# Kernel tuning notes

Measured on AMD Instinct MI355X. Metric: run time of the kernel, lower is better.

## Reference

```python
import jax, jax.numpy as jnp
import numpy as np

DIM = 512
N_HEADS = 8
HEAD_DIM = DIM // N_HEADS


def rope_pos(T, head_dim, dtype=jnp.float32):
    inv_freq = 1.0 / (10000.0 ** (jnp.arange(0, head_dim, 2, dtype=jnp.float32) / head_dim))
    t = jnp.arange(T, dtype=jnp.float32)
    freqs = jnp.einsum('i,j->ij', t, inv_freq)            # [T, head_dim/2]
    return jnp.concatenate([freqs, freqs], axis=-1).astype(dtype)  # [T, head_dim]


def rotate_half(x):
    x1, x2 = jnp.split(x, 2, axis=-1)
    return jnp.concatenate([-x2, x1], axis=-1)


def apply_rope(pos, t):
    # pos: [T, hd] -> broadcast to [1,1,T,hd]; t: [B,H,T,hd]
    pos = pos[None, None, :, :]
    return t * jnp.cos(pos) + rotate_half(t) * jnp.sin(pos)


def setup_inputs() -> dict:
    key = jax.random.key(0)
    ks = jax.random.split(key, 6)
    B, T = 4, 2048
    x = jax.random.normal(ks[0], (B, T, DIM), dtype=jnp.float32)
    mask = jnp.zeros((B, T), dtype=jnp.float32)  # additive mask
    s = 1.0 / np.sqrt(DIM)
    qkv_w = jax.random.normal(ks[1], (3 * DIM, DIM), dtype=jnp.float32) * s
    qkv_b = jnp.zeros((3 * DIM,), dtype=jnp.float32)
    proj_w = jax.random.normal(ks[2], (DIM, DIM), dtype=jnp.float32) * s
    proj_b = jnp.zeros((DIM,), dtype=jnp.float32)
    return {"x": x, "mask": mask, "qkv_w": qkv_w, "qkv_b": qkv_b,
            "proj_w": proj_w, "proj_b": proj_b}


def reference(x, mask, qkv_w, qkv_b, proj_w, proj_b):
    B, T, C = x.shape
    qkv = x @ qkv_w.T + qkv_b                       # [B,T,3C]
    qkv = qkv.reshape(B, T, 3, N_HEADS, HEAD_DIM)
    q, k, v = qkv[:, :, 0], qkv[:, :, 1], qkv[:, :, 2]  # [B,T,H,hd]
    q = q.transpose(0, 2, 1, 3)                     # [B,H,T,hd]
    k = k.transpose(0, 2, 1, 3)
    v = v.transpose(0, 2, 1, 3)
    pos = rope_pos(T, HEAD_DIM, x.dtype)
    q = apply_rope(pos, q)
    k = apply_rope(pos, k)
    scores = jnp.einsum('bhqd,bhkd->bhqk', q, k) * (1.0 / np.sqrt(HEAD_DIM))
    scores = scores + mask[:, None, None, :]        # 2D mask -> [B,1,1,T]
    probs = jax.nn.softmax(scores.astype(jnp.float32), axis=-1).astype(x.dtype)
    # dropout is identity in eval mode
    out = jnp.einsum('bhqk,bhkd->bhqd', probs, v)   # [B,H,T,hd]
    out = out.transpose(0, 2, 1, 3).reshape(B, T, C)
    return out @ proj_w.T + proj_b
```

## Files before the change

### kernel.cpp

```cpp
#include <hip/hip_runtime.h>
#include <math.h>


typedef __attribute__((ext_vector_type(8))) short bf16x8;
typedef __attribute__((ext_vector_type(4))) float floatx4;

#define LOG2E 1.44269504088896f

__device__ __forceinline__ unsigned short f2bf(float f) {
  unsigned int u = __float_as_uint(f);
  u += 0x7fffu + ((u >> 16) & 1u);
  return (unsigned short)(u >> 16);
}

__device__ __forceinline__ unsigned int cvtpk_bf16(float a, float b) {
  unsigned int r;
  asm("v_cvt_pk_bf16_f32 %0, %1, %2" : "=v"(r) : "v"(a), "v"(b));
  return r;
}

__device__ __forceinline__ void gld_lds16(unsigned short* lds, const unsigned short* g) {
  __builtin_amdgcn_global_load_lds(
      (const __attribute__((address_space(1))) unsigned int*)g,
      (__attribute__((address_space(3))) unsigned int*)lds, 16, 0, 0);
}

__global__ __launch_bounds__(256) void prep_kernel(
    const float* __restrict__ x, const float* __restrict__ wq, const float* __restrict__ wp,
    unsigned short* __restrict__ xb, unsigned short* __restrict__ wqb,
    unsigned short* __restrict__ wpb, float* __restrict__ cosT, float* __restrict__ sinT) {
  int i = blockIdx.x * 256 + threadIdx.x;
  if (i < 4194304) {
    xb[i] = f2bf(x[i]);
  } else if (i < 4980736) {
    int j = i - 4194304; wqb[j] = f2bf(wq[j]);
  } else if (i < 5242880) {
    int j = i - 4980736; wpb[j] = f2bf(wp[j]);
  } else if (i < 5308416) {
    int j = i - 5242880;
    int t = j >> 5, f = j & 31;
    double fr = (double)t * pow(10000.0, -(double)f / 32.0);
    cosT[j] = (float)cos(fr);
    sinT[j] = (float)sin(fr);
  }
}

__global__ __launch_bounds__(256) void qkv_kernel(
    const unsigned short* __restrict__ xb, const unsigned short* __restrict__ wqb,
    const float* __restrict__ qkv_b, const float* __restrict__ cosT,
    const float* __restrict__ sinT, unsigned short* __restrict__ Qb,
    unsigned short* __restrict__ Kb, unsigned short* __restrict__ Vtb) {
  __shared__ __align__(16) unsigned short As[128 * 32];
  __shared__ __align__(16) unsigned short Bs[128 * 32];
  const int tid = threadIdx.x;
  const int wave = tid >> 6, lane = tid & 63, ln = lane & 15, quad = lane >> 4;
  const int m0 = blockIdx.x * 128, n0 = blockIdx.y * 128;
  const int wr = (wave >> 1) * 64, wc = (wave & 1) * 64;

  floatx4 acc[4][4];
#pragma unroll
  for (int i = 0; i < 4; ++i)
#pragma unroll
    for (int j = 0; j < 4; ++j) acc[i][j] = (floatx4){0.f, 0.f, 0.f, 0.f};

  const int c0 = tid, c1 = tid + 256;
  const int ar0 = c0 >> 2, ak0 = (c0 & 3) * 8;
  const int ar1 = c1 >> 2, ak1 = (c1 & 3) * 8;

  for (int k0 = 0; k0 < 512; k0 += 32) {
    __syncthreads();
    gld_lds16(As + c0 * 8, xb + (size_t)(m0 + ar0) * 512 + k0 + ak0);
    gld_lds16(As + c1 * 8, xb + (size_t)(m0 + ar1) * 512 + k0 + ak1);
    gld_lds16(Bs + c0 * 8, wqb + (size_t)(n0 + ar0) * 512 + k0 + ak0);
    gld_lds16(Bs + c1 * 8, wqb + (size_t)(n0 + ar1) * 512 + k0 + ak1);
    __syncthreads();
    bf16x8 af[4], bfb[4];
#pragma unroll
    for (int mi = 0; mi < 4; ++mi)
      af[mi] = *(const bf16x8*)(As + (wr + mi * 16 + ln) * 32 + quad * 8);
#pragma unroll
    for (int ni = 0; ni < 4; ++ni)
      bfb[ni] = *(const bf16x8*)(Bs + (wc + ni * 16 + ln) * 32 + quad * 8);
#pragma unroll
    for (int mi = 0; mi < 4; ++mi)
#pragma unroll
      for (int ni = 0; ni < 4; ++ni)
        acc[mi][ni] = __builtin_amdgcn_mfma_f32_16x16x32_bf16(af[mi], bfb[ni], acc[mi][ni], 0, 0, 0);
  }

  const int colbase = n0 + wc;
  const int mat = colbase >> 9;
  const int h = (colbase & 511) >> 6;
  float bias[4];
#pragma unroll
  for (int ni = 0; ni < 4; ++ni) bias[ni] = qkv_b[colbase + ni * 16 + ln];

  if (mat == 2) {
#pragma unroll
    for (int mi = 0; mi < 4; ++mi) {
      int row0 = m0 + wr + mi * 16 + quad * 4;
      int bidx = row0 >> 11, t = row0 & 2047;
#pragma unroll
      for (int ni = 0; ni < 4; ++ni) {
        int d = ni * 16 + ln;
        ushort4 pk;
        pk.x = f2bf(acc[mi][ni][0] + bias[ni]);
        pk.y = f2bf(acc[mi][ni][1] + bias[ni]);
        pk.z = f2bf(acc[mi][ni][2] + bias[ni]);
        pk.w = f2bf(acc[mi][ni][3] + bias[ni]);
        *(ushort4*)(Vtb + ((size_t)(bidx * 8 + h) * 64 + d) * 2048 + t) = pk;
      }
    }
  } else {
    unsigned short* dst = (mat == 0) ? Qb : Kb;
    const float sc = (mat == 0) ? 0.125f * LOG2E : 1.0f;
#pragma unroll
    for (int mi = 0; mi < 4; ++mi) {
#pragma unroll
      for (int r = 0; r < 4; ++r) {
        int row = m0 + wr + mi * 16 + quad * 4 + r;
        int bidx = row >> 11, t = row & 2047;
        const float* cr = cosT + t * 32;
        const float* sr = sinT + t * 32;
        size_t obase = ((size_t)(bidx * 8 + h) * 2048 + t) * 64;
#pragma unroll
        for (int ni = 0; ni < 2; ++ni) {
          int dlo = ni * 16 + ln;
          float cv = cr[dlo], sv = sr[dlo];
          float xlo = acc[mi][ni][r] + bias[ni];
          float xhi = acc[mi][ni + 2][r] + bias[ni + 2];
          dst[obase + dlo]      = f2bf((xlo * cv - xhi * sv) * sc);
          dst[obase + dlo + 32] = f2bf((xhi * cv + xlo * sv) * sc);
        }
      }
    }
  }
}

__global__ __launch_bounds__(512) void attn_kernel(
    const unsigned short* __restrict__ Qb, const unsigned short* __restrict__ Kb,
    const unsigned short* __restrict__ Vtb, const float* __restrict__ mask,
    unsigned short* __restrict__ attnb) {
  __shared__ __align__(16) unsigned short Ks[64 * 64];
  __shared__ __align__(16) unsigned short Vs[64 * 64];
  __shared__ __align__(16) unsigned short Ps[128 * 64];

  const int tid = threadIdx.x;
  const int wave = tid >> 6, lane = tid & 63, ln = lane & 15, quad = lane >> 4;
  const int swz = (ln & 7) << 3;
  const int bh = blockIdx.y;
  const int b = bh >> 3, h = bh & 7;
  const int q0 = blockIdx.x * 128;
  const int wq = wave * 16;

  const unsigned short* Qhead = Qb + (size_t)bh * 2048 * 64;
  const unsigned short* Khead = Kb + (size_t)bh * 2048 * 64;
  const unsigned short* Vhead = Vtb + (size_t)bh * 64 * 2048;

  bf16x8 qf[2];
#pragma unroll
  for (int ks = 0; ks < 2; ++ks)
    qf[ks] = *(const bf16x8*)(Qhead + (size_t)(q0 + wq + ln) * 64 + ks * 32 + quad * 8);

  floatx4 o[4];
#pragma unroll
  for (int mi2 = 0; mi2 < 4; ++mi2) o[mi2] = (floatx4){0.f, 0.f, 0.f, 0.f};
  float mrun = -INFINITY;
  float lrun = 0.f;

  const int srow = tid >> 3;
  const int scol = (tid & 7) * 8;
  const int sdst = srow * 64 + (scol ^ ((srow & 7) << 3));
  uint4 kpre = *(const uint4*)(Khead + (size_t)srow * 64 + scol);
  uint4 vpre = *(const uint4*)(Vhead + (size_t)srow * 2048 + scol);

  for (int k0 = 0; k0 < 2048; k0 += 64) {
    __syncthreads();
    *(uint4*)(Ks + sdst) = kpre;
    *(uint4*)(Vs + sdst) = vpre;
    __syncthreads();
    if (k0 + 64 < 2048) {
      kpre = *(const uint4*)(Khead + (size_t)(k0 + 64 + srow) * 64 + scol);
      vpre = *(const uint4*)(Vhead + (size_t)srow * 2048 + k0 + 64 + scol);
    }

    floatx4 sm[4];
#pragma unroll
    for (int mi = 0; mi < 4; ++mi) {
      bf16x8 kf0 = *(const bf16x8*)(Ks + (mi * 16 + ln) * 64 + ((quad * 8) ^ swz));
      bf16x8 kf1 = *(const bf16x8*)(Ks + (mi * 16 + ln) * 64 + ((32 + quad * 8) ^ swz));
      floatx4 a = (floatx4){0.f, 0.f, 0.f, 0.f};
      a = __builtin_amdgcn_mfma_f32_16x16x32_bf16(kf0, qf[0], a, 0, 0, 0);
      a = __builtin_amdgcn_mfma_f32_16x16x32_bf16(kf1, qf[1], a, 0, 0, 0);
      sm[mi] = a;
    }
#pragma unroll
    for (int mi = 0; mi < 4; ++mi) {
      float4 mv = *(const float4*)(mask + b * 2048 + k0 + mi * 16 + quad * 4);
      sm[mi][0] += mv.x * LOG2E; sm[mi][1] += mv.y * LOG2E;
      sm[mi][2] += mv.z * LOG2E; sm[mi][3] += mv.w * LOG2E;
    }
    float vmax = fmaxf(fmaxf(sm[0][0], sm[0][1]), fmaxf(sm[0][2], sm[0][3]));
#pragma unroll
    for (int mi = 1; mi < 4; ++mi)
      vmax = fmaxf(vmax, fmaxf(fmaxf(sm[mi][0], sm[mi][1]), fmaxf(sm[mi][2], sm[mi][3])));
    vmax = fmaxf(vmax, __shfl_xor(vmax, 16));
    vmax = fmaxf(vmax, __shfl_xor(vmax, 32));
    if (__any(vmax > mrun)) {
      float nm = fmaxf(mrun, vmax);
      float alpha = exp2f(mrun - nm);
      mrun = nm;
      lrun *= alpha;
#pragma unroll
      for (int mi2 = 0; mi2 < 4; ++mi2) {
        o[mi2][0] *= alpha; o[mi2][1] *= alpha;
        o[mi2][2] *= alpha; o[mi2][3] *= alpha;
      }
    }
    float psum = 0.f;
#pragma unroll
    for (int mi = 0; mi < 4; ++mi)
#pragma unroll
      for (int r = 0; r < 4; ++r) {
        float p = exp2f(sm[mi][r] - mrun);
        sm[mi][r] = p;
        psum += p;
      }
    psum += __shfl_xor(psum, 16);
    psum += __shfl_xor(psum, 32);
    lrun += psum;

#pragma unroll
    for (int mi = 0; mi < 4; ++mi) {
      uint2 pk;
      pk.x = cvtpk_bf16(sm[mi][0], sm[mi][1]);
      pk.y = cvtpk_bf16(sm[mi][2], sm[mi][3]);
      *(uint2*)(Ps + (wq + ln) * 64 + ((mi * 16 + quad * 4) ^ swz)) = pk;
    }
#pragma unroll
    for (int ks = 0; ks < 2; ++ks) {
      bf16x8 pb = *(const bf16x8*)(Ps + (wq + ln) * 64 + ((ks * 32 + quad * 8) ^ swz));
#pragma unroll
      for (int mi2 = 0; mi2 < 4; ++mi2) {
        bf16x8 vf = *(const bf16x8*)(Vs + (mi2 * 16 + ln) * 64 + ((ks * 32 + quad * 8) ^ swz));
        o[mi2] = __builtin_amdgcn_mfma_f32_16x16x32_bf16(vf, pb, o[mi2], 0, 0, 0);
      }
    }
  }

  {
    float inv = 1.f / lrun;
    int t = q0 + wq + ln;
    size_t base = ((size_t)b * 2048 + t) * 512 + h * 64;
#pragma unroll
    for (int mi2 = 0; mi2 < 4; ++mi2) {
      uint2 pk;
      pk.x = cvtpk_bf16(o[mi2][0] * inv, o[mi2][1] * inv);
      pk.y = cvtpk_bf16(o[mi2][2] * inv, o[mi2][3] * inv);
      *(uint2*)(attnb + base + mi2 * 16 + quad * 4) = pk;
    }
  }
}

__global__ __launch_bounds__(256) void proj_kernel(
    const unsigned short* __restrict__ ab, const unsigned short* __restrict__ wpb,
    const float* __restrict__ proj_b, float* __restrict__ out) {
  __shared__ __align__(16) unsigned short As[128 * 32];
  __shared__ __align__(16) unsigned short Bs[128 * 32];
  const int tid = threadIdx.x;
  const int wave = tid >> 6, lane = tid & 63, ln = lane & 15, quad = lane >> 4;
  const int m0 = blockIdx.x * 128, n0 = blockIdx.y * 128;
  const int wr = (wave >> 1) * 64, wc = (wave & 1) * 64;

  floatx4 acc[4][4];
#pragma unroll
  for (int i = 0; i < 4; ++i)
#pragma unroll
    for (int j = 0; j < 4; ++j) acc[i][j] = (floatx4){0.f, 0.f, 0.f, 0.f};

  const int c0 = tid, c1 = tid + 256;
  const int ar0 = c0 >> 2, ak0 = (c0 & 3) * 8;
  const int ar1 = c1 >> 2, ak1 = (c1 & 3) * 8;

  for (int k0 = 0; k0 < 512; k0 += 32) {
    __syncthreads();
    gld_lds16(As + c0 * 8, ab + (size_t)(m0 + ar0) * 512 + k0 + ak0);
    gld_lds16(As + c1 * 8, ab + (size_t)(m0 + ar1) * 512 + k0 + ak1);
    gld_lds16(Bs + c0 * 8, wpb + (size_t)(n0 + ar0) * 512 + k0 + ak0);
    gld_lds16(Bs + c1 * 8, wpb + (size_t)(n0 + ar1) * 512 + k0 + ak1);
    __syncthreads();
    bf16x8 af[4], bfb[4];
#pragma unroll
    for (int mi = 0; mi < 4; ++mi)
      af[mi] = *(const bf16x8*)(As + (wr + mi * 16 + ln) * 32 + quad * 8);
#pragma unroll
    for (int ni = 0; ni < 4; ++ni)
      bfb[ni] = *(const bf16x8*)(Bs + (wc + ni * 16 + ln) * 32 + quad * 8);
#pragma unroll
    for (int mi = 0; mi < 4; ++mi)
#pragma unroll
      for (int ni = 0; ni < 4; ++ni)
        acc[mi][ni] = __builtin_amdgcn_mfma_f32_16x16x32_bf16(af[mi], bfb[ni], acc[mi][ni], 0, 0, 0);
  }

#pragma unroll
  for (int mi = 0; mi < 4; ++mi)
#pragma unroll
    for (int ni = 0; ni < 4; ++ni) {
      int col = n0 + wc + ni * 16 + ln;
      float pb = proj_b[col];
#pragma unroll
      for (int r = 0; r < 4; ++r) {
        int row = m0 + wr + mi * 16 + quad * 4 + r;
        out[(size_t)row * 512 + col] = acc[mi][ni][r] + pb;
      }
    }
}

extern "C" void kernel_launch(void* const* d_in, const int* in_sizes, int n_in,
                              void* d_out, int out_size, void* d_ws, size_t ws_size,
                              hipStream_t stream) {
  const float* x      = (const float*)d_in[0];
  const float* mask   = (const float*)d_in[1];
  const float* qkv_w  = (const float*)d_in[2];
  const float* qkv_b  = (const float*)d_in[3];
  const float* proj_w = (const float*)d_in[4];
  const float* proj_b = (const float*)d_in[5];
  float* out = (float*)d_out;

  char* ws = (char*)d_ws;
  unsigned short* xb   = (unsigned short*)(ws);
  unsigned short* wqb  = (unsigned short*)(ws + 8388608);
  unsigned short* wpb  = (unsigned short*)(ws + 9961472);
  float* cosT          = (float*)(ws + 10485760);
  float* sinT          = (float*)(ws + 10747904);
  unsigned short* Qb   = (unsigned short*)(ws + 11010048);
  unsigned short* Kb   = (unsigned short*)(ws + 19398656);
  unsigned short* Vtb  = (unsigned short*)(ws + 27787264);
  unsigned short* attnb= (unsigned short*)(ws + 36175872);

  prep_kernel<<<20736, 256, 0, stream>>>(x, qkv_w, proj_w, xb, wqb, wpb, cosT, sinT);
  dim3 g1(64, 12);
  qkv_kernel<<<g1, 256, 0, stream>>>(xb, wqb, qkv_b, cosT, sinT, Qb, Kb, Vtb);
  dim3 g2(16, 32);
  attn_kernel<<<g2, 512, 0, stream>>>(Qb, Kb, Vtb, mask, attnb);
  dim3 g3(64, 4);
  proj_kernel<<<g3, 256, 0, stream>>>(attnb, wpb, proj_b, out);
}
```

Before: 198.2 us.

## Split attention over two key halves and merge partials in a combine kernel

```diff
diff --git a/kernel.cpp b/kernel.cpp
--- a/kernel.cpp
+++ b/kernel.cpp
@@ -137,6 +137,165 @@
   }
 }
 
+__global__ __launch_bounds__(512) void attn_sk_kernel(
+    const unsigned short* __restrict__ Qb, const unsigned short* __restrict__ Kb,
+    const unsigned short* __restrict__ Vtb, const float* __restrict__ mask,
+    float* __restrict__ Opart, float* __restrict__ ml) {
+  __shared__ __align__(16) unsigned short Ks[64 * 64];
+  __shared__ __align__(16) unsigned short Vs[64 * 64];
+  __shared__ __align__(16) unsigned short Ps[128 * 64];
+
+  const int tid = threadIdx.x;
+  const int wave = tid >> 6, lane = tid & 63, ln = lane & 15, quad = lane >> 4;
+  const int swz = (ln & 7) << 3;
+  const int by = blockIdx.y;
+  const int bh = by >> 1, split = by & 1;
+  const int b = bh >> 3, h = bh & 7;
+  const int q0 = blockIdx.x * 128;
+  const int wq = wave * 16;
+  const int kbeg = split * 1024, kend = kbeg + 1024;
+  (void)h;
+
+  const unsigned short* Qhead = Qb + (size_t)bh * 2048 * 64;
+  const unsigned short* Khead = Kb + (size_t)bh * 2048 * 64;
+  const unsigned short* Vhead = Vtb + (size_t)bh * 64 * 2048;
+
+  bf16x8 qf[2];
+#pragma unroll
+  for (int ks = 0; ks < 2; ++ks)
+    qf[ks] = *(const bf16x8*)(Qhead + (size_t)(q0 + wq + ln) * 64 + ks * 32 + quad * 8);
+
+  floatx4 o[4];
+#pragma unroll
+  for (int mi2 = 0; mi2 < 4; ++mi2) o[mi2] = (floatx4){0.f, 0.f, 0.f, 0.f};
+  float mrun = -INFINITY;
+  float lrun = 0.f;
+
+  const int srow = tid >> 3;
+  const int scol = (tid & 7) * 8;
+  const int sdst = srow * 64 + (scol ^ ((srow & 7) << 3));
+  uint4 kpre = *(const uint4*)(Khead + (size_t)(kbeg + srow) * 64 + scol);
+  uint4 vpre = *(const uint4*)(Vhead + (size_t)srow * 2048 + kbeg + scol);
+
+  for (int k0 = kbeg; k0 < kend; k0 += 64) {
+    __syncthreads();
+    *(uint4*)(Ks + sdst) = kpre;
+    *(uint4*)(Vs + sdst) = vpre;
+    __syncthreads();
+    if (k0 + 64 < kend) {
+      kpre = *(const uint4*)(Khead + (size_t)(k0 + 64 + srow) * 64 + scol);
+      vpre = *(const uint4*)(Vhead + (size_t)srow * 2048 + k0 + 64 + scol);
+    }
+
+    floatx4 sm[4];
+#pragma unroll
+    for (int mi = 0; mi < 4; ++mi) {
+      bf16x8 kf0 = *(const bf16x8*)(Ks + (mi * 16 + ln) * 64 + ((quad * 8) ^ swz));
+      bf16x8 kf1 = *(const bf16x8*)(Ks + (mi * 16 + ln) * 64 + ((32 + quad * 8) ^ swz));
+      floatx4 a = (floatx4){0.f, 0.f, 0.f, 0.f};
+      a = __builtin_amdgcn_mfma_f32_16x16x32_bf16(kf0, qf[0], a, 0, 0, 0);
+      a = __builtin_amdgcn_mfma_f32_16x16x32_bf16(kf1, qf[1], a, 0, 0, 0);
+      sm[mi] = a;
+    }
+#pragma unroll
+    for (int mi = 0; mi < 4; ++mi) {
+      float4 mv = *(const float4*)(mask + b * 2048 + k0 + mi * 16 + quad * 4);
+      sm[mi][0] += mv.x * LOG2E; sm[mi][1] += mv.y * LOG2E;
+      sm[mi][2] += mv.z * LOG2E; sm[mi][3] += mv.w * LOG2E;
+    }
+    float vmax = fmaxf(fmaxf(sm[0][0], sm[0][1]), fmaxf(sm[0][2], sm[0][3]));
+#pragma unroll
+    for (int mi = 1; mi < 4; ++mi)
+      vmax = fmaxf(vmax, fmaxf(fmaxf(sm[mi][0], sm[mi][1]), fmaxf(sm[mi][2], sm[mi][3])));
+    vmax = fmaxf(vmax, __shfl_xor(vmax, 16));
+    vmax = fmaxf(vmax, __shfl_xor(vmax, 32));
+    if (__any(vmax > mrun)) {
+      float nm = fmaxf(mrun, vmax);
+      float alpha = exp2f(mrun - nm);
+      mrun = nm;
+      lrun *= alpha;
+#pragma unroll
+      for (int mi2 = 0; mi2 < 4; ++mi2) {
+        o[mi2][0] *= alpha; o[mi2][1] *= alpha;
+        o[mi2][2] *= alpha; o[mi2][3] *= alpha;
+      }
+    }
+    float psum = 0.f;
+#pragma unroll
+    for (int mi = 0; mi < 4; ++mi)
+#pragma unroll
+      for (int r = 0; r < 4; ++r) {
+        float p = exp2f(sm[mi][r] - mrun);
+        sm[mi][r] = p;
+        psum += p;
+      }
+    psum += __shfl_xor(psum, 16);
+    psum += __shfl_xor(psum, 32);
+    lrun += psum;
+
+#pragma unroll
+    for (int mi = 0; mi < 4; ++mi) {
+      uint2 pk;
+      pk.x = cvtpk_bf16(sm[mi][0], sm[mi][1]);
+      pk.y = cvtpk_bf16(sm[mi][2], sm[mi][3]);
+      *(uint2*)(Ps + (wq + ln) * 64 + ((mi * 16 + quad * 4) ^ swz)) = pk;
+    }
+#pragma unroll
+    for (int ks = 0; ks < 2; ++ks) {
+      bf16x8 pb = *(const bf16x8*)(Ps + (wq + ln) * 64 + ((ks * 32 + quad * 8) ^ swz));
+#pragma unroll
+      for (int mi2 = 0; mi2 < 4; ++mi2) {
+        bf16x8 vf = *(const bf16x8*)(Vs + (mi2 * 16 + ln) * 64 + ((ks * 32 + quad * 8) ^ swz));
+        o[mi2] = __builtin_amdgcn_mfma_f32_16x16x32_bf16(vf, pb, o[mi2], 0, 0, 0);
+      }
+    }
+  }
+
+  {
+    int t = q0 + wq + ln;
+    size_t qi = (size_t)bh * 2048 + t;
+    float* ob = Opart + ((size_t)split * 65536 + qi) * 64;
+#pragma unroll
+    for (int mi2 = 0; mi2 < 4; ++mi2)
+      *(floatx4*)(ob + mi2 * 16 + quad * 4) = o[mi2];
+    if (quad == 0) {
+      float2 v; v.x = mrun; v.y = lrun;
+      *(float2*)(ml + ((size_t)split * 65536 + qi) * 2) = v;
+    }
+  }
+}
+
+__global__ __launch_bounds__(256) void combine_kernel(
+    const float* __restrict__ Opart, const float* __restrict__ ml,
+    unsigned short* __restrict__ attnb) {
+  int g = blockIdx.x * 256 + threadIdx.x;
+  int qi = g >> 2, dq = (g & 3) * 16;
+  float2 a = *(const float2*)(ml + (size_t)qi * 2);
+  float2 c = *(const float2*)(ml + (size_t)(65536 + qi) * 2);
+  float m = fmaxf(a.x, c.x);
+  float w0 = exp2f(a.x - m), w1 = exp2f(c.x - m);
+  float inv = 1.f / (a.y * w0 + c.y * w1);
+  float s0 = w0 * inv, s1 = w1 * inv;
+  const float* p0 = Opart + (size_t)qi * 64 + dq;
+  const float* p1 = Opart + (size_t)(65536 + qi) * 64 + dq;
+  int bh = qi >> 11, t = qi & 2047, b = bh >> 3, h = bh & 7;
+  unsigned short* dst = attnb + ((size_t)b * 2048 + t) * 512 + h * 64 + dq;
+  unsigned int r[8];
+#pragma unroll
+  for (int j = 0; j < 4; ++j) {
+    float4 x0 = *(const float4*)(p0 + j * 4);
+    float4 x1 = *(const float4*)(p1 + j * 4);
+    float f0 = x0.x * s0 + x1.x * s1;
+    float f1 = x0.y * s0 + x1.y * s1;
+    float f2 = x0.z * s0 + x1.z * s1;
+    float f3 = x0.w * s0 + x1.w * s1;
+    r[2 * j]     = cvtpk_bf16(f0, f1);
+    r[2 * j + 1] = cvtpk_bf16(f2, f3);
+  }
+  *(uint4*)(dst)     = make_uint4(r[0], r[1], r[2], r[3]);
+  *(uint4*)(dst + 8) = make_uint4(r[4], r[5], r[6], r[7]);
+}
+
 __global__ __launch_bounds__(512) void attn_kernel(
     const unsigned short* __restrict__ Qb, const unsigned short* __restrict__ Kb,
     const unsigned short* __restrict__ Vtb, const float* __restrict__ mask,
@@ -338,12 +497,20 @@
   unsigned short* Kb   = (unsigned short*)(ws + 19398656);
   unsigned short* Vtb  = (unsigned short*)(ws + 27787264);
   unsigned short* attnb= (unsigned short*)(ws + 36175872);
+  float* Opart         = (float*)(ws + 44564480);
+  float* ml            = (float*)(ws + 78118912);
 
   prep_kernel<<<20736, 256, 0, stream>>>(x, qkv_w, proj_w, xb, wqb, wpb, cosT, sinT);
   dim3 g1(64, 12);
   qkv_kernel<<<g1, 256, 0, stream>>>(xb, wqb, qkv_b, cosT, sinT, Qb, Kb, Vtb);
-  dim3 g2(16, 32);
-  attn_kernel<<<g2, 512, 0, stream>>>(Qb, Kb, Vtb, mask, attnb);
+  if (ws_size >= 79167488) {
+    dim3 g2(16, 64);
+    attn_sk_kernel<<<g2, 512, 0, stream>>>(Qb, Kb, Vtb, mask, Opart, ml);
+    combine_kernel<<<1024, 256, 0, stream>>>(Opart, ml, attnb);
+  } else {
+    dim3 g2(16, 32);
+    attn_kernel<<<g2, 512, 0, stream>>>(Qb, Kb, Vtb, mask, attnb);
+  }
   dim3 g3(64, 4);
   proj_kernel<<<g3, 256, 0, stream>>>(attnb, wpb, proj_b, out);
 }
```

New measurement: 209.8 us. 1.06x slower.
